# Kernel tuning notes

Measured on AMD Instinct MI355X. Metric: run time of the kernel, lower is better.

Reference implementation:

```python
import jax, jax.numpy as jnp
import numpy as np

TEMPERATURE = 0.1
EPS = 1e-8  # torch CosineSimilarity eps


def _l2_normalize(x):
    # torch cosine sim: x / max(||x||, eps)
    n = jnp.sqrt(jnp.sum(x * x, axis=1, keepdims=True))
    return x / jnp.maximum(n, EPS)


def _pairwise_softmax(zx, zy):
    # cosine similarity matrix [N, N]: sim[i, j] = cos(zx[i], zy[j])
    sim = _l2_normalize(zx) @ _l2_normalize(zy).T  # [N, N]
    # softmax over dim=1 (columns) after temperature scaling
    return jax.nn.softmax(sim / TEMPERATURE, axis=1)


def _kl_div_mean(log_p, q):
    # torch F.kl_div(input=log_p, target=q, reduction='mean'):
    # mean over ALL elements of q * (log(q) - log_p)
    return jnp.mean(q * (jnp.log(q) - log_p))


def setup_inputs() -> dict:
    key = jax.random.key(0)
    k1, k2, k3, k4 = jax.random.split(key, 4)
    N, D = 4096, 768
    return {
        "zxs": jax.random.normal(k1, (N, D), dtype=jnp.float32),
        "zys": jax.random.normal(k2, (N, D), dtype=jnp.float32),
        "zxt": jax.random.normal(k3, (N, D), dtype=jnp.float32),
        "zyt": jax.random.normal(k4, (N, D), dtype=jnp.float32),
    }


def reference(zxs, zys, zxt, zyt):
    sim_s = _pairwise_softmax(zxs, zys)  # [N, N]
    sim_t = _pairwise_softmax(zxt, zyt)  # [N, N]
    loss_s = _kl_div_mean(jnp.log(sim_s), jax.lax.stop_gradient(sim_t))
    loss_t = _kl_div_mean(jnp.log(sim_t), jax.lax.stop_gradient(sim_s))
    return (loss_s, loss_t)
```

## Files before the change

kernel.cpp:

```cpp
#include <hip/hip_runtime.h>
#include <hip/hip_bf16.h>

#define N 4096
#define D 768
#define NC 6

typedef float f32x4 __attribute__((ext_vector_type(4)));
typedef int v8i __attribute__((ext_vector_type(8)));

typedef __attribute__((address_space(3))) unsigned int as3_uint;
typedef const __attribute__((address_space(1))) unsigned int as1_uint;

__device__ __forceinline__ void gload16(const void* g, void* l) {
    __builtin_amdgcn_global_load_lds((as1_uint*)g, (as3_uint*)l, 16, 0, 0);
}


__global__ __launch_bounds__(256) void norm4(const float* __restrict__ x0,
                                             const float* __restrict__ x1,
                                             const float* __restrict__ x2,
                                             const float* __restrict__ x3,
                                             unsigned char* __restrict__ o) {
    int a = blockIdx.y;
    const float* x = (a == 0) ? x0 : (a == 1) ? x1 : (a == 2) ? x2 : x3;
    unsigned char* out = o + (size_t)a * N * D;
    int i0 = blockIdx.x * 32;
    __shared__ __align__(16) unsigned char tile[24576];
    int t = threadIdx.x, lane = t & 63, w = t >> 6;

    for (int rr = 0; rr < 8; ++rr) {
        int R = i0 + w * 8 + rr;
        const f32x4* xr = (const f32x4*)(x + (size_t)R * D);
        f32x4 v0 = xr[lane * 2], v1 = xr[lane * 2 + 1];
        f32x4 v2 = {}, v3 = {};
        if (lane < 32) { v2 = xr[128 + lane * 2]; v3 = xr[128 + lane * 2 + 1]; }
        float ss = v0[0]*v0[0] + v0[1]*v0[1] + v0[2]*v0[2] + v0[3]*v0[3]
                 + v1[0]*v1[0] + v1[1]*v1[1] + v1[2]*v1[2] + v1[3]*v1[3]
                 + v2[0]*v2[0] + v2[1]*v2[1] + v2[2]*v2[2] + v2[3]*v2[3]
                 + v3[0]*v3[0] + v3[1]*v3[1] + v3[2]*v3[2] + v3[3]*v3[3];
        #pragma unroll
        for (int m = 1; m < 64; m <<= 1) ss += __shfl_xor(ss, m);
        float s = 1.0f / fmaxf(sqrtf(ss), 1e-8f);

        int lrg = (R >> 4) & 1;
        {
            unsigned int wlo = __builtin_amdgcn_cvt_pk_fp8_f32(v0[0]*s, v0[1]*s, 0, false) & 0xffff;
            unsigned int whi = __builtin_amdgcn_cvt_pk_fp8_f32(v0[2]*s, v0[3]*s, 0, false) & 0xffff;
            unsigned int w0 = wlo | (whi << 16);
            wlo = __builtin_amdgcn_cvt_pk_fp8_f32(v1[0]*s, v1[1]*s, 0, false) & 0xffff;
            whi = __builtin_amdgcn_cvt_pk_fp8_f32(v1[2]*s, v1[3]*s, 0, false) & 0xffff;
            unsigned int w1 = wlo | (whi << 16);
            int g = lane;
            int off = (lrg * 6 + (g >> 4)) * 2048 + ((g >> 1) & 1) * 1024
                    + ((R & 15) + 16 * ((g & 15) >> 2)) * 16 + (g & 1) * 8;
            *(uint2*)(tile + off) = make_uint2(w0, w1);
        }
        if (lane < 32) {
            unsigned int wlo = __builtin_amdgcn_cvt_pk_fp8_f32(v2[0]*s, v2[1]*s, 0, false) & 0xffff;
            unsigned int whi = __builtin_amdgcn_cvt_pk_fp8_f32(v2[2]*s, v2[3]*s, 0, false) & 0xffff;
            unsigned int w0 = wlo | (whi << 16);
            wlo = __builtin_amdgcn_cvt_pk_fp8_f32(v3[0]*s, v3[1]*s, 0, false) & 0xffff;
            whi = __builtin_amdgcn_cvt_pk_fp8_f32(v3[2]*s, v3[3]*s, 0, false) & 0xffff;
            unsigned int w1 = wlo | (whi << 16);
            int g = 64 + lane;
            int off = (lrg * 6 + (g >> 4)) * 2048 + ((g >> 1) & 1) * 1024
                    + ((R & 15) + 16 * ((g & 15) >> 2)) * 16 + (g & 1) * 8;
            *(uint2*)(tile + off) = make_uint2(w0, w1);
        }
    }
    __syncthreads();
    unsigned char* dst = out + (size_t)(i0 >> 5) * 24576;
    #pragma unroll
    for (int i = 0; i < 6; ++i)
        ((int4*)dst)[t + i * 256] = ((const int4*)tile)[t + i * 256];
}

__device__ __forceinline__ void gemm_pass(const unsigned char* __restrict__ A,
                                          const unsigned char* __restrict__ B,
                                          char* smem, int ib, int jb, int t,
                                          f32x4 (&acc)[4][4]) {
    const int lane = t & 63, w = t >> 6;
    const int wm = w >> 1, wn = w & 1;

    const unsigned char* gA = A + (size_t)((ib * 8 + 2 * w) * 6) * 2048 + lane * 16;
    const unsigned char* gB = B + (size_t)((jb * 8 + 2 * w) * 6) * 2048 + lane * 16;
    const int sd = w * 4096 + lane * 16;

    #define ISSUE(c)  do {                                                     \
        char* buf = smem + ((c) & 1) * 32768;                                  \
        const unsigned char* sa = gA + (c) * 2048;                             \
        const unsigned char* sb = gB + (c) * 2048;                             \
        gload16(sa,         buf + sd);                                         \
        gload16(sa + 1024,  buf + sd + 1024);                                  \
        gload16(sa + 12288, buf + sd + 2048);                                  \
        gload16(sa + 13312, buf + sd + 3072);                                  \
        gload16(sb,         buf + 16384 + sd);                                 \
        gload16(sb + 1024,  buf + 16384 + sd + 1024);                          \
        gload16(sb + 12288, buf + 16384 + sd + 2048);                          \
        gload16(sb + 13312, buf + 16384 + sd + 3072);                          \
    } while (0)

    ISSUE(0);

    #pragma unroll 1
    for (int c = 0; c < NC; ++c) {
        if (c < NC - 1) {
            ISSUE(c + 1);
            asm volatile("s_waitcnt vmcnt(8)" ::: "memory");
        } else {
            asm volatile("s_waitcnt vmcnt(0)" ::: "memory");
        }
        __builtin_amdgcn_s_barrier();
        asm volatile("" ::: "memory");

        const char* cb = smem + (c & 1) * 32768;
        union { int4 q[2]; v8i v; } a[4], b[4];
        #pragma unroll
        for (int m = 0; m < 4; ++m) {
            const char* p = cb + (wm * 4 + m) * 2048 + lane * 16;
            a[m].q[0] = *(const int4*)p;
            a[m].q[1] = *(const int4*)(p + 1024);
        }
        #pragma unroll
        for (int n = 0; n < 4; ++n) {
            const char* p = cb + 16384 + (wn * 4 + n) * 2048 + lane * 16;
            b[n].q[0] = *(const int4*)p;
            b[n].q[1] = *(const int4*)(p + 1024);
        }
        __builtin_amdgcn_s_setprio(1);
        #pragma unroll
        for (int m = 0; m < 4; ++m)
            #pragma unroll
            for (int n = 0; n < 4; ++n)
                acc[m][n] = __builtin_amdgcn_mfma_scale_f32_16x16x128_f8f6f4(
                    a[m].v, b[n].v, acc[m][n], 0, 0, 0, 127, 0, 127);
        __builtin_amdgcn_s_setprio(0);
        __builtin_amdgcn_s_barrier();
    }
    #undef ISSUE
}

__global__ __launch_bounds__(256, 2) void fused_gemm(
        const unsigned char* __restrict__ Xs, const unsigned char* __restrict__ Ys,
        const unsigned char* __restrict__ Xt, const unsigned char* __restrict__ Yt,
        float* __restrict__ partial) {
    __shared__ __align__(16) char smem[65536];
    const int t = threadIdx.x;
    const int bid = blockIdx.x;
    const int xcd = bid & 7, loc = bid >> 3;
    const int ib = (xcd >> 1) * 8 + (loc & 7);
    const int jb = (xcd & 1) * 16 + (loc >> 3);
    const int i0 = ib * 128;
    const int lane = t & 63, wid = t >> 6;
    const int wm = wid >> 1, wn = wid & 1;

    f32x4 acc_s[4][4] = {};
    f32x4 acc_t[4][4] = {};

    gemm_pass(Xs, Ys, smem, ib, jb, t, acc_s);
    gemm_pass(Xt, Yt, smem, ib, jb, t, acc_t);

    __syncthreads();
    float* p2 = (float*)smem;
    const int g = lane >> 4, cl = lane & 15;
    const int slot = wn * 16 + cl;

    #pragma unroll
    for (int m = 0; m < 4; ++m)
        #pragma unroll
        for (int r = 0; r < 4; ++r) {
            float e0 = 0.f, e1 = 0.f, e2 = 0.f, e3 = 0.f;
            #pragma unroll
            for (int n = 0; n < 4; ++n) {
                float ls = 10.0f * acc_s[m][n][r];
                float lt = 10.0f * acc_t[m][n][r];
                float es = __expf(ls - 10.0f);
                float et = __expf(lt - 10.0f);
                e0 += es;
                e1 += et;
                e2 += es * (ls - lt);
                e3 += et * (lt - ls);
            }
            int row = wm * 64 + m * 16 + g * 4 + r;
            int cell = row ^ (cl & 7);
            f32x4 vv = {e0, e1, e2, e3};
            *(f32x4*)(p2 + slot * 512 + cell * 4) = vv;
        }
    __syncthreads();

    {
        const int row = t >> 1, half = t & 1;
        f32x4 sum = {0.f, 0.f, 0.f, 0.f};
        #pragma unroll
        for (int j = 0; j < 16; ++j) {
            int sl = half * 16 + j;
            int cell = row ^ (sl & 7);
            sum += *(const f32x4*)(p2 + sl * 512 + cell * 4);
        }
        __syncthreads();
        *(f32x4*)(p2 + t * 4) = sum;
    }
    __syncthreads();
    #pragma unroll
    for (int q = 0; q < 2; ++q) {
        int idx2 = t + q * 256;
        int row = idx2 >> 2, s = idx2 & 3;
        float v = p2[(row * 2) * 4 + s] + p2[(row * 2 + 1) * 4 + s];
        partial[((size_t)jb * N + (i0 + row)) * 4 + s] = v;
    }
}

__global__ __launch_bounds__(256) void reduce_rows(const float* __restrict__ partial,
                                                   float* __restrict__ blocksum) {
    int row = blockIdx.x * 256 + threadIdx.x;
    float zs = 0.f, zt = 0.f, ws = 0.f, wt = 0.f;
    for (int jb = 0; jb < 32; ++jb) {
        const float* p = partial + ((size_t)jb * N + row) * 4;
        zs += p[0]; zt += p[1]; ws += p[2]; wt += p[3];
    }
    float ls_row = wt / zt - logf(zt) + logf(zs);
    float lt_row = ws / zs - logf(zs) + logf(zt);
    #pragma unroll
    for (int m = 1; m < 64; m <<= 1) {
        ls_row += __shfl_xor(ls_row, m);
        lt_row += __shfl_xor(lt_row, m);
    }
    __shared__ float rs[4], rt[4];
    int lane = threadIdx.x & 63, wid = threadIdx.x >> 6;
    if (lane == 0) { rs[wid] = ls_row; rt[wid] = lt_row; }
    __syncthreads();
    if (threadIdx.x == 0) {
        blocksum[blockIdx.x * 2]     = rs[0] + rs[1] + rs[2] + rs[3];
        blocksum[blockIdx.x * 2 + 1] = rt[0] + rt[1] + rt[2] + rt[3];
    }
}

__global__ void final_reduce(const float* __restrict__ blocksum, float* __restrict__ out) {
    float a = 0.f, b = 0.f;
    if (threadIdx.x < 16) { a = blocksum[threadIdx.x * 2]; b = blocksum[threadIdx.x * 2 + 1]; }
    #pragma unroll
    for (int m = 1; m < 16; m <<= 1) { a += __shfl_xor(a, m); b += __shfl_xor(b, m); }
    if (threadIdx.x == 0) {
        const float inv = 1.0f / 16777216.0f;
        out[0] = a * inv;
        out[1] = b * inv;
    }
}

extern "C" void kernel_launch(void* const* d_in, const int* in_sizes, int n_in,
                              void* d_out, int out_size, void* d_ws, size_t ws_size,
                              hipStream_t stream) {
    const float* zxs = (const float*)d_in[0];
    const float* zys = (const float*)d_in[1];
    const float* zxt = (const float*)d_in[2];
    const float* zyt = (const float*)d_in[3];

    char* ws = (char*)d_ws;
    const size_t A = (size_t)N * D;
    unsigned char* nb = (unsigned char*)ws;
    float* partial  = (float*)(ws + 4 * A);
    float* blocksum = (float*)(ws + 4 * A + (size_t)32 * N * 4 * sizeof(float));

    norm4<<<dim3(N / 32, 4), 256, 0, stream>>>(zxs, zys, zxt, zyt, nb);

    const unsigned char* Xs = nb;
    const unsigned char* Ys = nb + A;
    const unsigned char* Xt = nb + 2 * A;
    const unsigned char* Yt = nb + 3 * A;
    fused_gemm<<<dim3(1024), 256, 0, stream>>>(Xs, Ys, Xt, Yt, partial);

    reduce_rows<<<16, 256, 0, stream>>>(partial, blocksum);
    final_reduce<<<1, 64, 0, stream>>>(blocksum, (float*)d_out);
}
```

Measured before the change: 53.55 us.

## Prefetch teacher GEMM first chunk during student pass and reorder norm blocks

The GEMM pipeline now issues the first chunk of the teacher pass (Xt/Yt) into buffer 0 during the last iteration of the student pass. This removes the pipeline drain and refill bubble between the two passes. The normalization kernel also remaps blockIdx.x to row groups in a different order depending on the input index, likely so that rows needed early by GEMM blocks are written first or to spread memory traffic. The changes add index complexity, and correctness depends on buffer parity lining up, since NC is even and the last chunk sits in buffer 1.

Measured after the change: 51.64 us (median of 3 runs). -3.6%, faster.

```diff
diff --git a/kernel.cpp b/kernel.cpp
--- a/kernel.cpp
+++ b/kernel.cpp
@@ -24,7 +24,15 @@
     int a = blockIdx.y;
     const float* x = (a == 0) ? x0 : (a == 1) ? x1 : (a == 2) ? x2 : x3;
     unsigned char* out = o + (size_t)a * N * D;
-    int i0 = blockIdx.x * 32;
+    int xb = blockIdx.x;
+    int rg;
+    if (a & 1) {
+        rg = (xb & 1) * 64 + (xb >> 1);
+    } else {
+        int band = (xb & 7) >> 1;
+        rg = band * 32 + ((xb >> 3) << 1) + (xb & 1);
+    }
+    int i0 = rg * 32;
     __shared__ __align__(16) unsigned char tile[24576];
     int t = threadIdx.x, lane = t & 63, w = t >> 6;
 
@@ -69,7 +77,7 @@
         }
     }
     __syncthreads();
-    unsigned char* dst = out + (size_t)(i0 >> 5) * 24576;
+    unsigned char* dst = out + (size_t)rg * 24576;
     #pragma unroll
     for (int i = 0; i < 6; ++i)
         ((int4*)dst)[t + i * 256] = ((const int4*)tile)[t + i * 256];
@@ -77,19 +85,23 @@
 
 __device__ __forceinline__ void gemm_pass(const unsigned char* __restrict__ A,
                                           const unsigned char* __restrict__ B,
+                                          const unsigned char* __restrict__ An,
+                                          const unsigned char* __restrict__ Bn,
                                           char* smem, int ib, int jb, int t,
-                                          f32x4 (&acc)[4][4]) {
+                                          f32x4 (&acc)[4][4], bool first) {
     const int lane = t & 63, w = t >> 6;
     const int wm = w >> 1, wn = w & 1;
 
-    const unsigned char* gA = A + (size_t)((ib * 8 + 2 * w) * 6) * 2048 + lane * 16;
-    const unsigned char* gB = B + (size_t)((jb * 8 + 2 * w) * 6) * 2048 + lane * 16;
+    const size_t offA = (size_t)((ib * 8 + 2 * w) * 6) * 2048 + lane * 16;
+    const size_t offB = (size_t)((jb * 8 + 2 * w) * 6) * 2048 + lane * 16;
+    const unsigned char* gA = A + offA;
+    const unsigned char* gB = B + offB;
     const int sd = w * 4096 + lane * 16;
 
-    #define ISSUE(c)  do {                                                     \
-        char* buf = smem + ((c) & 1) * 32768;                                  \
-        const unsigned char* sa = gA + (c) * 2048;                             \
-        const unsigned char* sb = gB + (c) * 2048;                             \
+    #define ISSUE2(pA, pB, par, c)  do {                                       \
+        char* buf = smem + (par) * 32768;                                      \
+        const unsigned char* sa = (pA) + (c) * 2048;                           \
+        const unsigned char* sb = (pB) + (c) * 2048;                           \
         gload16(sa,         buf + sd);                                         \
         gload16(sa + 1024,  buf + sd + 1024);                                  \
         gload16(sa + 12288, buf + sd + 2048);                                  \
@@ -100,12 +112,17 @@
         gload16(sb + 13312, buf + 16384 + sd + 3072);                          \
     } while (0)
 
-    ISSUE(0);
+    if (first) ISSUE2(gA, gB, 0, 0);
 
     #pragma unroll 1
     for (int c = 0; c < NC; ++c) {
         if (c < NC - 1) {
-            ISSUE(c + 1);
+            ISSUE2(gA, gB, (c + 1) & 1, c + 1);
+            asm volatile("s_waitcnt vmcnt(8)" ::: "memory");
+        } else if (An != nullptr) {
+            const unsigned char* gAn = An + offA;
+            const unsigned char* gBn = Bn + offB;
+            ISSUE2(gAn, gBn, 0, 0);
             asm volatile("s_waitcnt vmcnt(8)" ::: "memory");
         } else {
             asm volatile("s_waitcnt vmcnt(0)" ::: "memory");
@@ -137,7 +154,7 @@
         __builtin_amdgcn_s_setprio(0);
         __builtin_amdgcn_s_barrier();
     }
-    #undef ISSUE
+    #undef ISSUE2
 }
 
 __global__ __launch_bounds__(256, 2) void fused_gemm(
@@ -157,8 +174,8 @@
     f32x4 acc_s[4][4] = {};
     f32x4 acc_t[4][4] = {};
 
-    gemm_pass(Xs, Ys, smem, ib, jb, t, acc_s);
-    gemm_pass(Xt, Yt, smem, ib, jb, t, acc_t);
+    gemm_pass(Xs, Ys, Xt, Yt, smem, ib, jb, t, acc_s, true);
+    gemm_pass(Xt, Yt, nullptr, nullptr, smem, ib, jb, t, acc_t, false);
 
     __syncthreads();
     float* p2 = (float*)smem;
```
